# Kernel optimization log

Measured on AMD Instinct MI355X. Metric: run time of the kernel, lower is better.

The kernel has to match this reference:

```python
import jax, jax.numpy as jnp
import numpy as np

B, S, H, D = 2, 2048, 16, 128
HID = H * D
ROPE_BASE = 10000.0


def _rope_tables(seq_len, dim, dtype):
    inv_freq = 1.0 / (ROPE_BASE ** (jnp.arange(0, dim, 2, dtype=jnp.float32) / dim))
    t = jnp.arange(seq_len, dtype=jnp.float32)
    freqs = jnp.einsum('s,d->sd', t, inv_freq)          # [S, D/2]
    emb = jnp.concatenate([freqs, freqs], axis=-1)       # [S, D]
    return jnp.cos(emb).astype(dtype), jnp.sin(emb).astype(dtype)


def _rotate_half(x):
    x1, x2 = jnp.split(x, 2, axis=-1)
    return jnp.concatenate([-x2, x1], axis=-1)


def _apply_rope(x, cos, sin, position_ids):
    # x: [B,H,S,D]; cos/sin: [S_emb, D]; position_ids: [B,S] or [1,S]
    c = cos[position_ids][:, None, :, :]  # [B,1,S,D]
    s = sin[position_ids][:, None, :, :]
    return x * c + _rotate_half(x) * s


def setup_inputs() -> dict:
    key = jax.random.key(0)
    ks = jax.random.split(key, 9)
    hidden_states = jax.random.normal(ks[0], (B, S, HID), jnp.float32) * 0.02
    Wq = jax.random.normal(ks[1], (HID, HID), jnp.float32) * 0.02
    Wk = jax.random.normal(ks[2], (HID, HID), jnp.float32) * 0.02
    Wv = jax.random.normal(ks[3], (HID, HID), jnp.float32) * 0.02
    Wo = jax.random.normal(ks[4], (HID, HID), jnp.float32) * 0.02
    # binary mask marking summary tokens
    sum_mask = jax.random.randint(ks[5], (B, S), 0, 2).astype(jnp.float32)
    # row-stochastic-ish averaging matrix over tokens (KV compression weights)
    raw = jax.random.uniform(ks[6], (B, S, S), jnp.float32)
    sum_attn_mask = sum_mask[:, :, None] * raw / jnp.sum(raw, axis=-1, keepdims=True)
    # additive causal mask [B,1,S,S]
    causal = jnp.tril(jnp.ones((S, S), dtype=bool))
    attention_mask = jnp.where(causal, 0.0, -1e9).astype(jnp.float32)
    attention_mask = jnp.broadcast_to(attention_mask[None, None], (B, 1, S, S))
    position_ids = jnp.broadcast_to(jnp.arange(S, dtype=jnp.int32), (B, S))
    return {
        'hidden_states': hidden_states, 'sum_mask': sum_mask,
        'sum_attn_mask': sum_attn_mask, 'attention_mask': attention_mask,
        'position_ids': position_ids, 'Wq': Wq, 'Wk': Wk, 'Wv': Wv, 'Wo': Wo,
    }


def reference(hidden_states, sum_mask, sum_attn_mask, attention_mask,
              position_ids, Wq, Wk, Wv, Wo):
    dtype = hidden_states.dtype
    # projections (F.linear: x @ W^T), then [B,H,S,D]
    def proj(W):
        return (hidden_states @ W.T).reshape(B, S, H, D).transpose(0, 2, 1, 3)
    q, k, v = proj(Wq), proj(Wk), proj(Wv)

    kv_seq_len = S
    cos, sin = _rope_tables(kv_seq_len, D, dtype)
    q = _apply_rope(q, cos, sin, position_ids)

    # KV compression: weighted token averaging injected at summary positions
    k_avg = jnp.einsum('bqk,bhkd->bhqd', sum_attn_mask, k)
    v_avg = jnp.einsum('bqk,bhkd->bhqd', sum_attn_mask, v)
    no_sum = (1.0 - sum_mask)[:, None, :, None]  # [B,1,S,1]
    k = no_sum * k + k_avg
    v = no_sum * v + v_avg

    key_pos = jnp.arange(kv_seq_len, dtype=jnp.int32)[None, :]  # [1,S]
    k = _apply_rope(k, cos, sin, key_pos)

    scale = 1.0 / np.sqrt(D)
    attn = jnp.einsum('bhqd,bhkd->bhqk', q, k) * scale
    attn = attn + attention_mask
    attn = jnp.maximum(attn, jnp.finfo(attn.dtype).min)
    attn = jax.nn.softmax(attn.astype(jnp.float32), axis=-1).astype(dtype)
    out = jnp.einsum('bhqk,bhkd->bhqd', attn, v)            # [B,H,S,D]
    out = out.transpose(0, 2, 1, 3).reshape(B, S, HID)
    return out @ Wo.T
```

## Files before the change

kernel.cpp:

```cpp
#include <hip/hip_runtime.h>
#include <cstdint>
#include <cstddef>

#define B_   2
#define S_   2048
#define H_   16
#define D_   128
#define HID_ 2048

typedef __bf16 bf16;
typedef unsigned short u16;
typedef bf16 bf16x4 __attribute__((ext_vector_type(4)));
typedef bf16 bf16x8 __attribute__((ext_vector_type(8)));
typedef u16  u16x8  __attribute__((ext_vector_type(8)));
typedef float f32x4 __attribute__((ext_vector_type(4)));

__device__ unsigned g_work;

__device__ __forceinline__ f32x4 mfma16(bf16x8 a, bf16x8 b, f32x4 c){
  return __builtin_amdgcn_mfma_f32_16x16x32_bf16(a, b, c, 0, 0, 0);
}

__device__ __forceinline__ void gload_lds16(const void* g, void* l){
  __builtin_amdgcn_global_load_lds((const __attribute__((address_space(1))) void*)g,
                                   (__attribute__((address_space(3))) void*)l, 16, 0, 0);
}

__device__ __forceinline__ void bar_lgkm(){
  asm volatile("s_waitcnt lgkmcnt(0)" ::: "memory");
  __builtin_amdgcn_s_barrier();
}
__device__ __forceinline__ void bar_full(){
  asm volatile("s_waitcnt vmcnt(0) lgkmcnt(0)" ::: "memory");
  __builtin_amdgcn_s_barrier();
}

__global__ void k_tables(float* __restrict__ cosT, float* __restrict__ sinT){
  if (blockIdx.x == 0 && threadIdx.x == 0) g_work = 0u;
  int id = blockIdx.x*256 + threadIdx.x;
  int p = id >> 6, i = id & 63;
  double f = (double)p * pow(10000.0, -(double)i/64.0);
  cosT[id] = (float)cos(f);
  sinT[id] = (float)sin(f);
}

__global__ void k_cvt_all(const float* __restrict__ a0, bf16* __restrict__ o0,
                          const float* __restrict__ a1, bf16* __restrict__ o1,
                          const float* __restrict__ w0, bf16* __restrict__ q0,
                          const float* __restrict__ w1, bf16* __restrict__ q1,
                          const float* __restrict__ w2, bf16* __restrict__ q2,
                          const float* __restrict__ w3, bf16* __restrict__ q3){
  const float* src; bf16* dst; int n4;
  switch (blockIdx.y){
    case 0: src = a0; dst = o0; n4 = 2097152; break;
    case 1: src = a1; dst = o1; n4 = 2097152; break;
    case 2: src = w0; dst = q0; n4 = 1048576; break;
    case 3: src = w1; dst = q1; n4 = 1048576; break;
    case 4: src = w2; dst = q2; n4 = 1048576; break;
    default: src = w3; dst = q3; n4 = 1048576; break;
  }
  int i = blockIdx.x*256 + threadIdx.x;
  if (i >= n4) return;
  f32x4 v = *reinterpret_cast<const f32x4*>(src + (size_t)i*4);
  bf16x4 o;
  o[0]=(bf16)v[0]; o[1]=(bf16)v[1]; o[2]=(bf16)v[2]; o[3]=(bf16)v[3];
  *reinterpret_cast<bf16x4*>(dst + (size_t)i*4) = o;
}

__global__ __launch_bounds__(256) void k_transpose_cvt(const float* __restrict__ in, bf16* __restrict__ out){
  __shared__ bf16 t[64][72];
  const int tid = threadIdx.x;
  const int b = blockIdx.z, j0 = blockIdx.x*64, s0 = blockIdx.y*64;
  #pragma unroll
  for (int u0 = 0; u0 < 4; ++u0){
    int u = u0*256 + tid;
    int r = u >> 4, c4 = (u & 15)*4;
    f32x4 v = *reinterpret_cast<const f32x4*>(in + ((size_t)b*S_ + s0 + r)*HID_ + j0 + c4);
    bf16x4 o; o[0]=(bf16)v[0]; o[1]=(bf16)v[1]; o[2]=(bf16)v[2]; o[3]=(bf16)v[3];
    *reinterpret_cast<bf16x4*>(&t[r][c4]) = o;
  }
  __syncthreads();
  #pragma unroll
  for (int u0 = 0; u0 < 4; ++u0){
    int u = u0*256 + tid;
    int r = u >> 4, c4 = (u & 15)*4;
    bf16x4 o;
    o[0] = t[c4+0][r]; o[1] = t[c4+1][r]; o[2] = t[c4+2][r]; o[3] = t[c4+3][r];
    *reinterpret_cast<bf16x4*>(out + ((size_t)b*HID_ + j0 + r)*S_ + s0 + c4) = o;
  }
}

template<int EPI>
__global__ __launch_bounds__(256) void k_gemm_nt(
    const bf16* __restrict__ A, const bf16* __restrict__ Bm, void* __restrict__ Cv,
    int Kd, size_t sAz, size_t sBz, size_t sCz, int N,
    const float* __restrict__ mask, const float* __restrict__ hid)
{
  const int tid = threadIdx.x;
  const int wid = tid >> 6, lane = tid & 63;
  const int g = lane >> 4, li = lane & 15;
  const int z = blockIdx.z;
  const int m0 = blockIdx.y*128, n0 = blockIdx.x*128;
  const int wm = wid >> 1, wn = wid & 1;
  const bf16* Ab = A + (size_t)z*sAz;
  const bf16* Bb = Bm + (size_t)z*sBz;

  __shared__ bf16 lA[128*64];
  __shared__ bf16 lB[128*64];

  f32x4 acc[4][4];
  #pragma unroll
  for (int i=0;i<4;++i)
    #pragma unroll
    for (int j=0;j<4;++j)
      acc[i][j] = {0.f,0.f,0.f,0.f};

  for (int k0 = 0; k0 < Kd; k0 += 64){
    #pragma unroll
    for (int j=0;j<4;++j){
      int ci = j*256 + tid;
      int r = ci >> 3, cb = ci & 7;
      gload_lds16(Ab + (size_t)(m0 + r)*Kd + k0 + cb*8, (char*)lA + (j*256 + wid*64)*16);
      gload_lds16(Bb + (size_t)(n0 + r)*Kd + k0 + cb*8, (char*)lB + (j*256 + wid*64)*16);
    }
    __syncthreads();
    #pragma unroll
    for (int kk=0;kk<2;++kk){
      bf16x8 af[4], bfm[4];
      #pragma unroll
      for (int i=0;i<4;++i){
        af[i]  = *reinterpret_cast<const bf16x8*>(&lA[(wm*64 + i*16 + li)*64 + kk*32 + g*8]);
        bfm[i] = *reinterpret_cast<const bf16x8*>(&lB[(wn*64 + i*16 + li)*64 + kk*32 + g*8]);
      }
      #pragma unroll
      for (int i=0;i<4;++i)
        #pragma unroll
        for (int j=0;j<4;++j)
          acc[i][j] = mfma16(af[i], bfm[j], acc[i][j]);
    }
    __syncthreads();
  }

  #pragma unroll
  for (int i=0;i<4;++i){
    #pragma unroll
    for (int j=0;j<4;++j){
      #pragma unroll
      for (int v=0;v<4;++v){
        int row = m0 + wm*64 + i*16 + g*4 + v;
        int col = n0 + wn*64 + j*16 + li;
        float x = acc[i][j][v];
        if (EPI == 1){
          x += (1.f - mask[z*S_ + row]) * hid[((size_t)z*S_ + row)*HID_ + col];
          ((bf16*)Cv)[(size_t)z*sCz + (size_t)row*N + col] = (bf16)x;
        } else if (EPI == 0){
          ((bf16*)Cv)[(size_t)row*N + col] = (bf16)x;
        } else if (EPI == 2){
          ((float*)Cv)[(size_t)row*N + col] = x;
        } else {
          if (n0 < 2048) ((bf16*)Cv)[(size_t)row*2048 + col] = (bf16)x;
          else ((bf16*)(void*)hid)[(size_t)row*2048 + col - 2048] = (bf16)x;
        }
      }
    }
  }
}

template<int EPI>
__global__ __launch_bounds__(512,2) void k_gemm256(
    const bf16* __restrict__ A, const bf16* __restrict__ Bm, void* __restrict__ Cv,
    int Kd, size_t sAz, size_t sBz, size_t sCz, int N,
    const float* __restrict__ mask, const float* __restrict__ hid)
{
  const int tid = threadIdx.x;
  const int wid = tid >> 6, lane = tid & 63;
  const int g = lane >> 4, li = lane & 15;
  const int wm = wid >> 2, wn = wid & 3;
  const int z = blockIdx.z;
  const int m0 = blockIdx.y*256, n0 = blockIdx.x*256;
  const bf16* Ab = A + (size_t)z*sAz + (size_t)m0*Kd;
  const bf16* Bb = Bm + (size_t)z*sBz + (size_t)n0*Kd;

  __shared__ bf16 lA[2][256*64];
  __shared__ bf16 lB[2][256*64];

  const int rr0 = tid >> 3, cc = tid & 7;
  const int rr1 = rr0 + 64;
  const int cx0 = cc ^ (rr0 & 7);
  const int cx1 = cc ^ (rr1 & 7);

  f32x4 acc[8][4];
  #pragma unroll
  for (int i=0;i<8;++i)
    #pragma unroll
    for (int j=0;j<4;++j) acc[i][j] = {0.f,0.f,0.f,0.f};

  auto stage = [&](int buf, int kt, int matsel, int half){
    const bf16* s = matsel ? Bb : Ab;
    char* dbase = (char*)(matsel ? lB[buf] : lA[buf]) + half*16384;
    gload_lds16(s + (size_t)(half*128 + rr0)*Kd + kt*64 + cx0*8, dbase + (wid*64)*16);
    gload_lds16(s + (size_t)(half*128 + rr1)*Kd + kt*64 + cx1*8, dbase + (512 + wid*64)*16);
  };
  auto rdA = [&](int buf, int i, int kh){
    int row = wm*128 + i*16 + li;
    return *reinterpret_cast<const bf16x8*>((const char*)lA[buf] + row*128 + (((kh*4 + g) ^ (row & 7))*16));
  };
  auto rdB = [&](int buf, int j, int kh){
    int row = wn*64 + j*16 + li;
    return *reinterpret_cast<const bf16x8*>((const char*)lB[buf] + row*128 + (((kh*4 + g) ^ (row & 7))*16));
  };

  const int NT = Kd >> 6;
  stage(0,0,0,0); stage(0,0,0,1); stage(0,0,1,0); stage(0,0,1,1);
  __syncthreads();

  int cur = 0;
  for (int kt = 0; kt < NT; ++kt){
    const bool more = (kt+1 < NT);
    bf16x8 af[4], bfr[4];

    if (more){
      stage(cur^1, kt+1, 0, 0); stage(cur^1, kt+1, 0, 1);
      stage(cur^1, kt+1, 1, 0); stage(cur^1, kt+1, 1, 1);
    }
    #pragma unroll
    for (int i=0;i<4;++i) af[i] = rdA(cur, i, 0);
    #pragma unroll
    for (int j=0;j<4;++j) bfr[j] = rdB(cur, j, 0);
    __builtin_amdgcn_s_setprio(1);
    #pragma unroll
    for (int i=0;i<4;++i)
      #pragma unroll
      for (int j=0;j<4;++j) acc[i][j] = mfma16(af[i], bfr[j], acc[i][j]);
    __builtin_amdgcn_s_setprio(0);
    __builtin_amdgcn_s_barrier();

    #pragma unroll
    for (int i=0;i<4;++i) af[i] = rdA(cur, i+4, 0);
    __builtin_amdgcn_s_setprio(1);
    #pragma unroll
    for (int i=0;i<4;++i)
      #pragma unroll
      for (int j=0;j<4;++j) acc[i+4][j] = mfma16(af[i], bfr[j], acc[i+4][j]);
    __builtin_amdgcn_s_setprio(0);
    __builtin_amdgcn_s_barrier();

    #pragma unroll
    for (int i=0;i<4;++i) af[i] = rdA(cur, i, 1);
    #pragma unroll
    for (int j=0;j<4;++j) bfr[j] = rdB(cur, j, 1);
    __builtin_amdgcn_s_setprio(1);
    #pragma unroll
    for (int i=0;i<4;++i)
      #pragma unroll
      for (int j=0;j<4;++j) acc[i][j] = mfma16(af[i], bfr[j], acc[i][j]);
    __builtin_amdgcn_s_setprio(0);
    __builtin_amdgcn_s_barrier();

    #pragma unroll
    for (int i=0;i<4;++i) af[i] = rdA(cur, i+4, 1);
    __builtin_amdgcn_s_setprio(1);
    #pragma unroll
    for (int i=0;i<4;++i)
      #pragma unroll
      for (int j=0;j<4;++j) acc[i+4][j] = mfma16(af[i], bfr[j], acc[i+4][j]);
    __builtin_amdgcn_s_setprio(0);

    __syncthreads();
    cur ^= 1;
  }

  #pragma unroll
  for (int i=0;i<8;++i){
    #pragma unroll
    for (int j=0;j<4;++j){
      #pragma unroll
      for (int v=0;v<4;++v){
        int row = m0 + wm*128 + i*16 + g*4 + v;
        int col = n0 + wn*64 + j*16 + li;
        float x = acc[i][j][v];
        if (EPI == 1){
          x += (1.f - mask[z*S_ + row]) * hid[((size_t)z*S_ + row)*HID_ + col];
          ((bf16*)Cv)[(size_t)z*sCz + (size_t)row*N + col] = (bf16)x;
        } else if (EPI == 0){
          ((bf16*)Cv)[(size_t)row*N + col] = (bf16)x;
        } else if (EPI == 2){
          ((float*)Cv)[(size_t)row*N + col] = x;
        } else {
          if (n0 < 2048) ((bf16*)Cv)[(size_t)row*2048 + col] = (bf16)x;
          else ((bf16*)(void*)hid)[(size_t)row*2048 + col - 2048] = (bf16)x;
        }
      }
    }
  }
}

__global__ void k_rope(bf16* __restrict__ X, const float* __restrict__ cosT,
                       const float* __restrict__ sinT, const int* __restrict__ pos){
  int id = blockIdx.x*256 + threadIdx.x;
  int d4 = (id & 15)*4;
  int h  = (id >> 4) & 15;
  int s  = (id >> 8) & 2047;
  int b  = id >> 19;
  int p = pos ? pos[b*S_ + s] : s;
  size_t base = (((size_t)b*S_ + s)*H_ + h)*D_ + d4;
  f32x4 c  = *reinterpret_cast<const f32x4*>(cosT + (size_t)p*64 + d4);
  f32x4 sn = *reinterpret_cast<const f32x4*>(sinT + (size_t)p*64 + d4);
  bf16x4 x1 = *reinterpret_cast<bf16x4*>(X + base);
  bf16x4 x2 = *reinterpret_cast<bf16x4*>(X + base + 64);
  bf16x4 o1, o2;
  #pragma unroll
  for (int i=0;i<4;++i){
    float a = (float)x1[i], bb = (float)x2[i];
    o1[i] = (bf16)(a*c[i] - bb*sn[i]);
    o2[i] = (bf16)(bb*c[i] + a*sn[i]);
  }
  *reinterpret_cast<bf16x4*>(X + base) = o1;
  *reinterpret_cast<bf16x4*>(X + base + 64) = o2;
}

__global__ __launch_bounds__(256,2) void k_flash(const bf16* __restrict__ Q, const bf16* __restrict__ K,
                                                 const bf16* __restrict__ V, bf16* __restrict__ O,
                                                 float* __restrict__ OP, float* __restrict__ ML)
{
  const int tid = threadIdx.x;
  const int wid = tid >> 6, lane = tid & 63;
  const int g = lane >> 4, li = lane & 15;

  __shared__ bf16 Klds[2][64*128];
  __shared__ char VtB[128*128];
  __shared__ bf16 Plds[4][32*72];
  __shared__ int s_item;

  const int dc0 = tid & 15, kvp0 = tid >> 4;
  const int kvp1 = kvp0 + 16;

  for (;;) {
    if (tid == 0) s_item = (int)atomicAdd(&g_work, 1u);
    __syncthreads();
    const int w = s_item;
    if (w >= 672) return;

    int qx, bh, part, t0, t1;
    if (w < 96)       { qx = 10 - (w >> 5);  bh = w & 31;  part = -1; t0 = 0; t1 = 2*qx + 2; }
    else if (w < 416) { int u = w - 96;  qx = 15 - (u >> 6); int r = u & 63; bh = r >> 1; part = r & 1;
                        int nt = 2*qx + 2, mid = nt >> 1; t0 = part ? mid : 0; t1 = part ? nt : mid; }
    else              { int u = w - 416; qx = 7 - (u >> 5);  bh = u & 31;  part = -1; t0 = 0; t1 = 2*qx + 2; }

    const int qb = qx * 128;
    const size_t headoff = ((size_t)(bh >> 4)*S_*H_ + (bh & 15))*D_;
    const bf16* Kh = K + headoff;
    const u16*  Vh = (const u16*)(V + headoff);

    bf16x8 qf[2][4];
    #pragma unroll
    for (int rb=0;rb<2;++rb){
      const bf16* Qp = Q + headoff + (size_t)(qb + wid*32 + rb*16 + li)*H_*D_;
      #pragma unroll
      for (int kc=0;kc<4;++kc)
        qf[rb][kc] = *reinterpret_cast<const bf16x8*>(Qp + kc*32 + g*8);
    }

    float mrun[2][4], lrun[2][4];
    f32x4 acc[2][8];
    #pragma unroll
    for (int rb=0;rb<2;++rb){
      #pragma unroll
      for (int v=0;v<4;++v){ mrun[rb][v] = -1e30f; lrun[rb][v] = 0.f; }
      #pragma unroll
      for (int fn=0;fn<8;++fn) acc[rb][fn] = {0.f,0.f,0.f,0.f};
    }

    u16x8 vp[4];
    auto stageK = [&](int buf, int t){
      #pragma unroll
      for (int j=0;j<4;++j){
        int ci = j*256 + tid;
        int r = ci >> 4, cb = ci & 15;
        const char* src = (const char*)(Kh + (size_t)(t*64 + r)*H_*D_) + ((cb ^ (r & 7)) * 16);
        gload_lds16(src, (char*)Klds[buf] + (j*256 + wid*64)*16);
      }
    };
    auto loadV = [&](int t){
      const u16* s0p = Vh + (size_t)(t*64 + kvp0*2)*H_*D_ + dc0*8;
      const u16* s1p = Vh + (size_t)(t*64 + kvp1*2)*H_*D_ + dc0*8;
      vp[0] = *reinterpret_cast<const u16x8*>(s0p);
      vp[1] = *reinterpret_cast<const u16x8*>(s0p + H_*D_);
      vp[2] = *reinterpret_cast<const u16x8*>(s1p);
      vp[3] = *reinterpret_cast<const u16x8*>(s1p + H_*D_);
    };
    auto writeVtB = [&](){
      #pragma unroll
      for (int j=0;j<2;++j){
        int kvp = j ? kvp1 : kvp0;
        #pragma unroll
        for (int e=0;e<8;++e){
          int r = dc0*8 + e;
          int swz = (r ^ (r >> 3)) & 7;
          int addr = r*128 + (((kvp >> 2) ^ swz) << 4) + ((kvp << 2) & 12);
          *reinterpret_cast<uint32_t*>(VtB + addr) =
              (uint32_t)vp[j*2+0][e] | ((uint32_t)vp[j*2+1][e] << 16);
        }
      }
    };

    stageK(0, t0);
    loadV(t0);
    writeVtB();
    bar_full();

    int cur = 0;
    for (int t=t0; t<t1; ++t){
      const bool more = (t+1 < t1);
      if (more){ stageK(cur^1, t+1); loadV(t+1); }

      f32x4 sc[2][4];
      #pragma unroll
      for (int fc=0;fc<4;++fc){
        int r = fc*16 + li;
        bf16x8 kf[4];
        #pragma unroll
        for (int kc=0;kc<4;++kc)
          kf[kc] = *reinterpret_cast<const bf16x8*>((const char*)Klds[cur] + r*256 + (((4*kc + g) ^ (r & 7))*16));
        __builtin_amdgcn_s_setprio(1);
        #pragma unroll
        for (int rb=0;rb<2;++rb){
          f32x4 s = {0.f,0.f,0.f,0.f};
          #pragma unroll
          for (int kc=0;kc<4;++kc)
            s = mfma16(qf[rb][kc], kf[kc], s);
          sc[rb][fc] = s;
        }
        __builtin_amdgcn_s_setprio(0);
      }

      const float scale = 0.08838834764831845f;
      const int c0 = t*64;
      if (t >= 2*qx){
        #pragma unroll
        for (int rb=0;rb<2;++rb){
          const int rowg = qb + wid*32 + rb*16 + g*4;
          #pragma unroll
          for (int fc=0;fc<4;++fc){
            int col = c0 + fc*16 + li;
            #pragma unroll
            for (int v=0;v<4;++v){
              float s = sc[rb][fc][v] * scale;
              sc[rb][fc][v] = (col > rowg + v) ? -1e30f : s;
            }
          }
        }
      } else {
        #pragma unroll
        for (int rb=0;rb<2;++rb)
          #pragma unroll
          for (int fc=0;fc<4;++fc)
            #pragma unroll
            for (int v=0;v<4;++v)
              sc[rb][fc][v] *= scale;
      }

      #pragma unroll
      for (int rb=0;rb<2;++rb){
        float tm[4];
        #pragma unroll
        for (int v=0;v<4;++v){
          float m2 = fmaxf(fmaxf(sc[rb][0][v], sc[rb][1][v]), fmaxf(sc[rb][2][v], sc[rb][3][v]));
          m2 = fmaxf(m2, __shfl_xor(m2, 1));
          m2 = fmaxf(m2, __shfl_xor(m2, 2));
          m2 = fmaxf(m2, __shfl_xor(m2, 4));
          m2 = fmaxf(m2, __shfl_xor(m2, 8));
          tm[v] = m2;
        }
        bool need = false;
        #pragma unroll
        for (int v=0;v<4;++v) need = need || (tm[v] > mrun[rb][v] + 8.f);
        if (__any(need)){
          float al[4];
          #pragma unroll
          for (int v=0;v<4;++v){
            float mnew = fmaxf(mrun[rb][v], tm[v]);
            al[v] = __expf(mrun[rb][v] - mnew);
            mrun[rb][v] = mnew;
            lrun[rb][v] *= al[v];
          }
          #pragma unroll
          for (int fn=0;fn<8;++fn)
            #pragma unroll
            for (int v=0;v<4;++v) acc[rb][fn][v] *= al[v];
        }
        float rs[4] = {0.f,0.f,0.f,0.f};
        #pragma unroll
        for (int fc=0;fc<4;++fc){
          #pragma unroll
          for (int v=0;v<4;++v){
            float p = __expf(sc[rb][fc][v] - mrun[rb][v]);
            rs[v] += p;
            Plds[wid][(rb*16 + g*4 + v)*72 + fc*16 + li] = (bf16)p;
          }
        }
        #pragma unroll
        for (int v=0;v<4;++v){
          float r = rs[v];
          r += __shfl_xor(r, 1); r += __shfl_xor(r, 2);
          r += __shfl_xor(r, 4); r += __shfl_xor(r, 8);
          lrun[rb][v] += r;
        }
      }

      bf16x8 pa[2][2];
      #pragma unroll
      for (int rb=0;rb<2;++rb)
        #pragma unroll
        for (int kc=0;kc<2;++kc)
          pa[rb][kc] = *reinterpret_cast<const bf16x8*>(&Plds[wid][(rb*16 + li)*72 + kc*32 + g*8]);
      #pragma unroll
      for (int fn=0;fn<8;++fn){
        int r = fn*16 + li;
        int swz = (r ^ (r >> 3)) & 7;
        bf16x8 bv[2];
        #pragma unroll
        for (int kc=0;kc<2;++kc)
          bv[kc] = *reinterpret_cast<const bf16x8*>(VtB + r*128 + (((kc*4 + g) ^ swz) << 4));
        __builtin_amdgcn_s_setprio(1);
        #pragma unroll
        for (int rb=0;rb<2;++rb)
          #pragma unroll
          for (int kc=0;kc<2;++kc)
            acc[rb][fn] = mfma16(pa[rb][kc], bv[kc], acc[rb][fn]);
        __builtin_amdgcn_s_setprio(0);
      }

      if (more){
        bar_lgkm();
        writeVtB();
      }
      bar_full();
      cur ^= 1;
    }

    if (part < 0){
      #pragma unroll
      for (int rb=0;rb<2;++rb){
        #pragma unroll
        for (int v=0;v<4;++v){
          float inv = 1.f / lrun[rb][v];
          int row = qb + wid*32 + rb*16 + g*4 + v;
          bf16* dst = O + headoff + (size_t)row*H_*D_ + li;
          #pragma unroll
          for (int fn=0;fn<8;++fn)
            dst[fn*16] = (bf16)(acc[rb][fn][v] * inv);
        }
      }
    } else {
      const int sidx = (15 - qx)*64 + (bh << 1) + part;
      float* Od = OP + (size_t)sidx*128*128;
      #pragma unroll
      for (int rb=0;rb<2;++rb){
        #pragma unroll
        for (int v=0;v<4;++v){
          int rl = wid*32 + rb*16 + g*4 + v;
          #pragma unroll
          for (int fn=0;fn<8;++fn)
            Od[rl*128 + fn*16 + li] = acc[rb][fn][v];
          if (li == 0){
            ML[(size_t)sidx*256 + rl*2 + 0] = mrun[rb][v];
            ML[(size_t)sidx*256 + rl*2 + 1] = lrun[rb][v];
          }
        }
      }
    }
  }
}

__global__ __launch_bounds__(256) void k_merge(const float* __restrict__ OP, const float* __restrict__ ML,
                                               bf16* __restrict__ O){
  const int pair = blockIdx.x;
  const int qi = pair >> 5;
  const int qx = 15 - qi;
  const int bh = pair & 31;
  const int s0 = qi*64 + (bh << 1), s1 = s0 + 1;
  const int b = bh >> 4, h = bh & 15;
  const int qb = qx * 128;
  const int row = threadIdx.x >> 1;
  const int cseg = (threadIdx.x & 1) * 64;

  float m0 = ML[(size_t)s0*256 + row*2], l0 = ML[(size_t)s0*256 + row*2 + 1];
  float m1 = ML[(size_t)s1*256 + row*2], l1 = ML[(size_t)s1*256 + row*2 + 1];
  float m = fmaxf(m0, m1);
  float e0 = __expf(m0 - m), e1 = __expf(m1 - m);
  float inv = 1.f / (l0*e0 + l1*e1);
  const float* O0 = OP + ((size_t)s0*128 + row)*128 + cseg;
  const float* O1 = OP + ((size_t)s1*128 + row)*128 + cseg;
  bf16* dst = O + (((size_t)b*S_ + qb + row)*H_ + h)*D_ + cseg;
  #pragma unroll
  for (int c=0; c<64; c+=4){
    f32x4 a = *reinterpret_cast<const f32x4*>(O0 + c);
    f32x4 bb = *reinterpret_cast<const f32x4*>(O1 + c);
    bf16x4 o;
    #pragma unroll
    for (int i=0;i<4;++i) o[i] = (bf16)((a[i]*e0 + bb[i]*e1) * inv);
    *reinterpret_cast<bf16x4*>(dst + c) = o;
  }
}

extern "C" void kernel_launch(void* const* d_in, const int* in_sizes, int n_in,
                              void* d_out, int out_size, void* d_ws, size_t ws_size,
                              hipStream_t stream)
{
  (void)in_sizes; (void)n_in; (void)out_size; (void)ws_size;
  const float* hid   = (const float*)d_in[0];
  const float* smask = (const float*)d_in[1];
  const float* samat = (const float*)d_in[2];
  const int*   pos   = (const int*)d_in[4];
  const float* Wq = (const float*)d_in[5];
  const float* Wk = (const float*)d_in[6];
  const float* Wv = (const float*)d_in[7];
  const float* Wo = (const float*)d_in[8];
  float* out = (float*)d_out;
  char* ws = (char*)d_ws;

  const size_t SZ_TAB = (size_t)S_*64*4;
  const size_t SZ_BSH = (size_t)B_*S_*HID_*2;
  float* cosT = (float*)(ws);
  float* sinT = (float*)(ws + SZ_TAB);
  bf16* buf1 = (bf16*)(ws + 2*SZ_TAB);
  bf16* buf2 = (bf16*)(ws + 2*SZ_TAB + 1*SZ_BSH);
  bf16* buf3 = (bf16*)(ws + 2*SZ_TAB + 2*SZ_BSH);
  bf16* buf4 = (bf16*)(ws + 2*SZ_TAB + 3*SZ_BSH);
  bf16* Wqb = (bf16*)(ws + 2*SZ_TAB + 4*SZ_BSH);
  bf16* Wkb = Wqb + (size_t)HID_*HID_;
  bf16* Wvb = Wkb + (size_t)HID_*HID_;
  bf16* Wob = Wvb + (size_t)HID_*HID_;
  float* OP = (float*)Wqb;
  float* ML = OP + (size_t)320*128*128;

  k_tables<<<512,256,0,stream>>>(cosT, sinT);
  k_cvt_all<<<dim3(8192,6),256,0,stream>>>(hid, buf1, samat, buf3,
                                           Wq, Wqb, Wk, Wkb, Wv, Wvb, Wo, Wob);
  k_transpose_cvt<<<dim3(32,32,2),256,0,stream>>>(hid, buf2);

  const size_t sBat = (size_t)S_*HID_;
  k_gemm_nt<1><<<dim3(16,16,2),256,0,stream>>>(buf3, buf2, buf4, 2048, sBat, sBat, sBat, 2048, smask, hid);
  k_gemm_nt<0><<<dim3(16,32,1),256,0,stream>>>(buf1, Wqb, buf3, 2048, 0,0,0, 2048, nullptr, nullptr);
  k_rope<<<4096,256,0,stream>>>(buf3, cosT, sinT, pos);
  k_gemm256<3><<<dim3(16,16,1),512,0,stream>>>(buf4, Wkb, buf2, 2048, 0,0,0, 2048, nullptr, (const float*)buf1);
  k_rope<<<4096,256,0,stream>>>(buf2, cosT, sinT, nullptr);
  k_flash<<<dim3(512),256,0,stream>>>(buf3, buf2, buf1, buf4, OP, ML);
  k_merge<<<dim3(160),256,0,stream>>>(OP, ML, buf4);
  k_gemm_nt<2><<<dim3(16,32,1),256,0,stream>>>(buf4, Wob, out, 2048, 0,0,0, 2048, nullptr, nullptr);
}
```

Before: 427.3 us.

## Double flash-attention query tile to 256 rows with 512-thread blocks

```diff
diff --git a/kernel.cpp b/kernel.cpp
--- a/kernel.cpp
+++ b/kernel.cpp
@@ -319,9 +319,9 @@
   *reinterpret_cast<bf16x4*>(X + base + 64) = o2;
 }
 
-__global__ __launch_bounds__(256,2) void k_flash(const bf16* __restrict__ Q, const bf16* __restrict__ K,
+__global__ __launch_bounds__(512,2) void k_flash(const bf16* __restrict__ Q, const bf16* __restrict__ K,
                                                  const bf16* __restrict__ V, bf16* __restrict__ O,
-                                                 float* __restrict__ OP, float* __restrict__ ML)
+                                                 bf16* __restrict__ OPb, float* __restrict__ ML)
 {
   const int tid = threadIdx.x;
   const int wid = tid >> 6, lane = tid & 63;
@@ -329,25 +329,28 @@
 
   __shared__ bf16 Klds[2][64*128];
   __shared__ char VtB[128*128];
-  __shared__ bf16 Plds[4][32*72];
+  __shared__ bf16 Plds[8][32*72];
   __shared__ int s_item;
 
-  const int dc0 = tid & 15, kvp0 = tid >> 4;
-  const int kvp1 = kvp0 + 16;
+  const int dc = tid & 15, kvp = tid >> 4;
 
   for (;;) {
     if (tid == 0) s_item = (int)atomicAdd(&g_work, 1u);
     __syncthreads();
     const int w = s_item;
-    if (w >= 672) return;
+    if (w >= 384) return;
 
     int qx, bh, part, t0, t1;
-    if (w < 96)       { qx = 10 - (w >> 5);  bh = w & 31;  part = -1; t0 = 0; t1 = 2*qx + 2; }
-    else if (w < 416) { int u = w - 96;  qx = 15 - (u >> 6); int r = u & 63; bh = r >> 1; part = r & 1;
-                        int nt = 2*qx + 2, mid = nt >> 1; t0 = part ? mid : 0; t1 = part ? nt : mid; }
-    else              { int u = w - 416; qx = 7 - (u >> 5);  bh = u & 31;  part = -1; t0 = 0; t1 = 2*qx + 2; }
-
-    const int qb = qx * 128;
+    if (w < 64)       { qx = 7; int u = w;       bh = u>>1; part = u&1; t0 = part?16:0; t1 = part?32:16; }
+    else if (w < 96)  { qx = 3; bh = w-64;  part = -1; t0 = 0; t1 = 16; }
+    else if (w < 160) { qx = 6; int u = w-96;  bh = u>>1; part = u&1; t0 = part?14:0; t1 = part?28:14; }
+    else if (w < 224) { qx = 5; int u = w-160; bh = u>>1; part = u&1; t0 = part?12:0; t1 = part?24:12; }
+    else if (w < 256) { qx = 2; bh = w-224; part = -1; t0 = 0; t1 = 12; }
+    else if (w < 320) { qx = 4; int u = w-256; bh = u>>1; part = u&1; t0 = part?10:0; t1 = part?20:10; }
+    else if (w < 352) { qx = 1; bh = w-320; part = -1; t0 = 0; t1 = 8; }
+    else              { qx = 0; bh = w-352; part = -1; t0 = 0; t1 = 4; }
+
+    const int qb = qx * 256;
     const size_t headoff = ((size_t)(bh >> 4)*S_*H_ + (bh & 15))*D_;
     const bf16* Kh = K + headoff;
     const u16*  Vh = (const u16*)(V + headoff);
@@ -371,36 +374,29 @@
       for (int fn=0;fn<8;++fn) acc[rb][fn] = {0.f,0.f,0.f,0.f};
     }
 
-    u16x8 vp[4];
+    u16x8 vp[2];
     auto stageK = [&](int buf, int t){
       #pragma unroll
-      for (int j=0;j<4;++j){
-        int ci = j*256 + tid;
+      for (int j=0;j<2;++j){
+        int ci = j*512 + tid;
         int r = ci >> 4, cb = ci & 15;
         const char* src = (const char*)(Kh + (size_t)(t*64 + r)*H_*D_) + ((cb ^ (r & 7)) * 16);
-        gload_lds16(src, (char*)Klds[buf] + (j*256 + wid*64)*16);
+        gload_lds16(src, (char*)Klds[buf] + (j*512 + wid*64)*16);
       }
     };
     auto loadV = [&](int t){
-      const u16* s0p = Vh + (size_t)(t*64 + kvp0*2)*H_*D_ + dc0*8;
-      const u16* s1p = Vh + (size_t)(t*64 + kvp1*2)*H_*D_ + dc0*8;
-      vp[0] = *reinterpret_cast<const u16x8*>(s0p);
-      vp[1] = *reinterpret_cast<const u16x8*>(s0p + H_*D_);
-      vp[2] = *reinterpret_cast<const u16x8*>(s1p);
-      vp[3] = *reinterpret_cast<const u16x8*>(s1p + H_*D_);
+      const u16* sp = Vh + (size_t)(t*64 + kvp*2)*H_*D_ + dc*8;
+      vp[0] = *reinterpret_cast<const u16x8*>(sp);
+      vp[1] = *reinterpret_cast<const u16x8*>(sp + H_*D_);
     };
     auto writeVtB = [&](){
       #pragma unroll
-      for (int j=0;j<2;++j){
-        int kvp = j ? kvp1 : kvp0;
-        #pragma unroll
-        for (int e=0;e<8;++e){
-          int r = dc0*8 + e;
-          int swz = (r ^ (r >> 3)) & 7;
-          int addr = r*128 + (((kvp >> 2) ^ swz) << 4) + ((kvp << 2) & 12);
-          *reinterpret_cast<uint32_t*>(VtB + addr) =
-              (uint32_t)vp[j*2+0][e] | ((uint32_t)vp[j*2+1][e] << 16);
-        }
+      for (int e=0;e<8;++e){
+        int r = dc*8 + e;
+        int swz = (r ^ (r >> 3)) & 7;
+        int addr = r*128 + (((kvp >> 2) ^ swz) << 4) + ((kvp << 2) & 12);
+        *reinterpret_cast<uint32_t*>(VtB + addr) =
+            (uint32_t)vp[0][e] | ((uint32_t)vp[1][e] << 16);
       }
     };
 
@@ -436,7 +432,7 @@
 
       const float scale = 0.08838834764831845f;
       const int c0 = t*64;
-      if (t >= 2*qx){
+      if (t >= 4*qx){
         #pragma unroll
         for (int rb=0;rb<2;++rb){
           const int rowg = qb + wid*32 + rb*16 + g*4;
@@ -553,19 +549,21 @@
         }
       }
     } else {
-      const int sidx = (15 - qx)*64 + (bh << 1) + part;
-      float* Od = OP + (size_t)sidx*128*128;
+      const int sidx = ((qx-4)<<6) + (bh<<1) + part;
+      bf16* Od = OPb + (size_t)sidx*256*128;
+      float* MLd = ML + (size_t)sidx*512;
       #pragma unroll
       for (int rb=0;rb<2;++rb){
         #pragma unroll
         for (int v=0;v<4;++v){
+          float inv = 1.f / lrun[rb][v];
           int rl = wid*32 + rb*16 + g*4 + v;
           #pragma unroll
           for (int fn=0;fn<8;++fn)
-            Od[rl*128 + fn*16 + li] = acc[rb][fn][v];
+            Od[rl*128 + fn*16 + li] = (bf16)(acc[rb][fn][v] * inv);
           if (li == 0){
-            ML[(size_t)sidx*256 + rl*2 + 0] = mrun[rb][v];
-            ML[(size_t)sidx*256 + rl*2 + 1] = lrun[rb][v];
+            MLd[rl*2 + 0] = mrun[rb][v];
+            MLd[rl*2 + 1] = lrun[rb][v];
           }
         }
       }
@@ -573,34 +571,33 @@
   }
 }
 
-__global__ __launch_bounds__(256) void k_merge(const float* __restrict__ OP, const float* __restrict__ ML,
+__global__ __launch_bounds__(256) void k_merge(const bf16* __restrict__ OPb, const float* __restrict__ ML,
                                                bf16* __restrict__ O){
-  const int pair = blockIdx.x;
-  const int qi = pair >> 5;
-  const int qx = 15 - qi;
-  const int bh = pair & 31;
-  const int s0 = qi*64 + (bh << 1), s1 = s0 + 1;
+  const int gid = blockIdx.x;
+  const int qx = 4 + (gid >> 5);
+  const int bh = gid & 31;
+  const int s0 = ((qx-4)<<6) + (bh<<1), s1 = s0 + 1;
   const int b = bh >> 4, h = bh & 15;
-  const int qb = qx * 128;
-  const int row = threadIdx.x >> 1;
-  const int cseg = (threadIdx.x & 1) * 64;
-
-  float m0 = ML[(size_t)s0*256 + row*2], l0 = ML[(size_t)s0*256 + row*2 + 1];
-  float m1 = ML[(size_t)s1*256 + row*2], l1 = ML[(size_t)s1*256 + row*2 + 1];
-  float m = fmaxf(m0, m1);
-  float e0 = __expf(m0 - m), e1 = __expf(m1 - m);
-  float inv = 1.f / (l0*e0 + l1*e1);
-  const float* O0 = OP + ((size_t)s0*128 + row)*128 + cseg;
-  const float* O1 = OP + ((size_t)s1*128 + row)*128 + cseg;
-  bf16* dst = O + (((size_t)b*S_ + qb + row)*H_ + h)*D_ + cseg;
-  #pragma unroll
-  for (int c=0; c<64; c+=4){
-    f32x4 a = *reinterpret_cast<const f32x4*>(O0 + c);
-    f32x4 bb = *reinterpret_cast<const f32x4*>(O1 + c);
-    bf16x4 o;
-    #pragma unroll
-    for (int i=0;i<4;++i) o[i] = (bf16)((a[i]*e0 + bb[i]*e1) * inv);
-    *reinterpret_cast<bf16x4*>(dst + c) = o;
+  const int qb = qx * 256;
+  const int row = threadIdx.x;
+
+  float m0 = ML[(size_t)s0*512 + row*2], l0 = ML[(size_t)s0*512 + row*2 + 1];
+  float m1 = ML[(size_t)s1*512 + row*2], l1 = ML[(size_t)s1*512 + row*2 + 1];
+  float mm = fmaxf(m0, m1);
+  float w0 = l0 * __expf(m0 - mm), w1 = l1 * __expf(m1 - mm);
+  float inv = 1.f / (w0 + w1);
+  w0 *= inv; w1 *= inv;
+  const bf16* r0 = OPb + ((size_t)s0*256 + row)*128;
+  const bf16* r1 = OPb + ((size_t)s1*256 + row)*128;
+  bf16* dst = O + (((size_t)b*S_ + qb + row)*H_ + h)*D_;
+  #pragma unroll
+  for (int c=0; c<128; c+=8){
+    bf16x8 a = *reinterpret_cast<const bf16x8*>(r0 + c);
+    bf16x8 bq = *reinterpret_cast<const bf16x8*>(r1 + c);
+    bf16x8 o;
+    #pragma unroll
+    for (int i=0;i<8;++i) o[i] = (bf16)((float)a[i]*w0 + (float)bq[i]*w1);
+    *reinterpret_cast<bf16x8*>(dst + c) = o;
   }
 }
 
@@ -632,8 +629,8 @@
   bf16* Wkb = Wqb + (size_t)HID_*HID_;
   bf16* Wvb = Wkb + (size_t)HID_*HID_;
   bf16* Wob = Wvb + (size_t)HID_*HID_;
-  float* OP = (float*)Wqb;
-  float* ML = OP + (size_t)320*128*128;
+  bf16* OPb = Wqb;
+  float* ML = (float*)(Wqb + (size_t)256*256*128);
 
   k_tables<<<512,256,0,stream>>>(cosT, sinT);
   k_cvt_all<<<dim3(8192,6),256,0,stream>>>(hid, buf1, samat, buf3,
@@ -646,7 +643,7 @@
   k_rope<<<4096,256,0,stream>>>(buf3, cosT, sinT, pos);
   k_gemm256<3><<<dim3(16,16,1),512,0,stream>>>(buf4, Wkb, buf2, 2048, 0,0,0, 2048, nullptr, (const float*)buf1);
   k_rope<<<4096,256,0,stream>>>(buf2, cosT, sinT, nullptr);
-  k_flash<<<dim3(512),256,0,stream>>>(buf3, buf2, buf1, buf4, OP, ML);
-  k_merge<<<dim3(160),256,0,stream>>>(OP, ML, buf4);
+  k_flash<<<dim3(256),512,0,stream>>>(buf3, buf2, buf1, buf4, OPb, ML);
+  k_merge<<<dim3(128),256,0,stream>>>(OPb, ML, buf4);
   k_gemm_nt<2><<<dim3(16,32,1),256,0,stream>>>(buf4, Wob, out, 2048, 0,0,0, 2048, nullptr, nullptr);
 }
```

New measurement: 413.8 us. -3.1%, faster.
